# Optimization experiments

Hardware: AMD Instinct MI355X
Metric: run time of the kernel (lower is better)

## Reference

```python
import jax, jax.numpy as jnp
import numpy as np


def setup_inputs() -> dict:
    key = jax.random.key(0)
    ks = jax.random.split(key, 5)
    B, Cin, Ch, H, W, K = 8, 64, 64, 128, 128, 3
    fan_in = (Cin + Ch) * K * K
    return {
        "x": jax.random.normal(ks[0], (B, Cin, H, W), jnp.float32),
        "prev_h": jax.random.normal(ks[1], (B, Ch, H, W), jnp.float32),
        "prev_c": jax.random.normal(ks[2], (B, Ch, H, W), jnp.float32),
        "W_gates": jax.random.normal(ks[3], (4 * Ch, Cin + Ch, K, K), jnp.float32) / np.sqrt(fan_in),
        "b_gates": jax.random.normal(ks[4], (4 * Ch,), jnp.float32) * 0.01,
    }


def reference(x, prev_h, prev_c, W_gates, b_gates):
    # ConvLSTM cell: conv over concat(input, prev_h) -> 4 gates -> gating.
    pad = W_gates.shape[-1] // 2
    stacked = jnp.concatenate([x, prev_h], axis=1)  # [B, Cin+Ch, H, W]
    gates = jax.lax.conv_general_dilated(
        stacked, W_gates,
        window_strides=(1, 1),
        padding=[(pad, pad), (pad, pad)],
        dimension_numbers=("NCHW", "OIHW", "NCHW"),
    ) + b_gates[None, :, None, None]  # [B, 4*Ch, H, W]
    in_gate, remember_gate, out_gate, cell_gate = jnp.split(gates, 4, axis=1)
    in_gate = jax.nn.sigmoid(in_gate)
    remember_gate = jax.nn.sigmoid(remember_gate)
    out_gate = jax.nn.sigmoid(out_gate)
    cell_gate = jnp.tanh(cell_gate)
    cell = in_gate * cell_gate + remember_gate * prev_c
    hidden = out_gate * jnp.tanh(cell)
    return (hidden, cell)
```

## Files before the change

kernel.cpp:

```cpp
#include <hip/hip_runtime.h>

typedef __attribute__((ext_vector_type(8))) short short8;
typedef __attribute__((ext_vector_type(4))) short short4v;
typedef __attribute__((ext_vector_type(4))) float float4v;

#define NPIX_HID 8388608
#define PST 132

__device__ __forceinline__ short f2bf(float f) {
    union { float f; unsigned u; } v; v.f = f;
    unsigned r = (v.u + 0x7FFFu + ((v.u >> 16) & 1u)) >> 16;
    return (short)r;
}

__device__ __forceinline__ float sigmoidf_(float v) { return 1.f / (1.f + __expf(-v)); }
__device__ __forceinline__ float tanhf_(float v)    { return 2.f / (1.f + __expf(-2.f * v)) - 1.f; }

__global__ void wprep(const float* __restrict__ W, short* __restrict__ A) {
    int tid = blockIdx.x * 256 + threadIdx.x;
    if (tid >= 9 * 16 * 256 * 8) return;
    int j   = tid & 7;
    int co  = (tid >> 3) & 255;
    int cig = (tid >> 11) & 15;
    int kk  = tid >> 15;
    int ci  = cig * 8 + j;
    A[tid] = f2bf(W[co * 1152 + ci * 9 + kk]);
}

#define ST_LOAD(P, II)                                                        \
  {                                                                           \
    const int i_ = (II);                                                      \
    P##_act = (i_ < 4224);                                                    \
    const int px_ = i_ % 66;                                                  \
    const int ro_ = i_ / 66;                                                  \
    P##_oct = ro_ & 15;                                                       \
    P##_row = ro_ >> 4;                                                       \
    const int ys_ = y0 + P##_row - 1;                                         \
    const int xs_ = x0 + px_ - 1;                                             \
    P##_px = px_;                                                             \
    P##_ok = P##_act & ((unsigned)ys_ < 128u) & ((unsigned)xs_ < 128u);       \
    const float* src_ = (P##_oct < 8) ? x : ph;                               \
    const float* sp_ = src_ + (P##_ok ?                                       \
        (((b * 64 + (P##_oct & 7) * 8) * 128 + ys_) * 128 + xs_) : 0);        \
    P##_v[0] = sp_[0];        P##_v[1] = sp_[16384];                          \
    P##_v[2] = sp_[2 * 16384]; P##_v[3] = sp_[3 * 16384];                     \
    P##_v[4] = sp_[4 * 16384]; P##_v[5] = sp_[5 * 16384];                     \
    P##_v[6] = sp_[6 * 16384]; P##_v[7] = sp_[7 * 16384];                     \
  }

#define ST_PROC(P)                                                            \
  if (P##_act) {                                                              \
    short4v lo_ = {0,0,0,0}, hi_ = {0,0,0,0};                                 \
    if (P##_ok) {                                                             \
      lo_[0] = f2bf(P##_v[0]); lo_[1] = f2bf(P##_v[1]);                       \
      lo_[2] = f2bf(P##_v[2]); lo_[3] = f2bf(P##_v[3]);                       \
      hi_[0] = f2bf(P##_v[4]); hi_[1] = f2bf(P##_v[5]);                       \
      hi_[2] = f2bf(P##_v[6]); hi_[3] = f2bf(P##_v[7]);                       \
    }                                                                         \
    short* dst_ = &Bs[(P##_row * 66 + P##_px) * PST + P##_oct * 8];           \
    *(short4v*)dst_       = lo_;                                              \
    *(short4v*)(dst_ + 4) = hi_;                                              \
  }

__global__ __launch_bounds__(256, 2) void convlstm_main(
    const float* __restrict__ x, const float* __restrict__ ph,
    const float* __restrict__ pc, const short* __restrict__ aprep,
    const float* __restrict__ bg, float* __restrict__ out)
{
    __shared__ short Bs[4 * 66 * PST];

    const int tid  = threadIdx.x;
    const int lane = tid & 63;
    const int wave = tid >> 6;
    const int l15  = lane & 15;
    const int quad = lane >> 4;

    const int t  = (blockIdx.x & 7) * 128 + (blockIdx.x >> 3);
    const int x0 = (t & 1) * 64;
    const int y0 = ((t >> 1) & 63) * 2;
    const int b  = t >> 7;

    {
        float stA_v[8]; int stA_px, stA_row, stA_oct; bool stA_ok, stA_act;
        float stB_v[8]; int stB_px, stB_row, stB_oct; bool stB_ok, stB_act;
        int ib = tid;
        ST_LOAD(stA, ib);
#pragma unroll 1
        for (int it = 0; it < 16; it += 2) {
            ST_LOAD(stB, ib + 256);
            ST_PROC(stA);
            ST_LOAD(stA, ib + 512);
            ST_PROC(stB);
            ib += 512;
        }
        ST_PROC(stA);
    }
    __syncthreads();

    float4v acc[4][8];
#pragma unroll
    for (int mt = 0; mt < 4; ++mt)
#pragma unroll
        for (int nt = 0; nt < 8; ++nt)
            acc[mt][nt] = (float4v){0.f, 0.f, 0.f, 0.f};

    const short* ap = aprep + quad * 2048 + (wave * 16 + l15) * 8;
    short8 abuf[2][4];
#pragma unroll
    for (int mt = 0; mt < 4; ++mt) abuf[0][mt] = *(const short8*)(ap + mt * 512);

    const short* bb = &Bs[l15 * PST + quad * 8];
    short8 bfr[2][8];
#pragma unroll
    for (int nt = 0; nt < 8; ++nt) {
        const short* bp = bb + (nt >> 2) * (66 * PST) + (nt & 3) * (16 * PST);
        short4v lo = *(const short4v*)bp;
        short4v hi = *(const short4v*)(bp + 4);
        bfr[0][nt] = __builtin_shufflevector(lo, hi, 0, 1, 2, 3, 4, 5, 6, 7);
    }

#pragma unroll 1
    for (int ky = 0; ky < 3; ++ky) {
#pragma unroll 1
        for (int kx = 0; kx < 3; ++kx) {
            const bool lastkx = (ky == 2) & (kx == 2);
            const short* bbn = bb + ((kx == 2) ? 64 * PST : PST);
#pragma unroll
            for (int kc = 0; kc < 4; ++kc) {
                const int cur = kc & 1, nxt = cur ^ 1;
                const bool last = lastkx & (kc == 3);

                const short* apn = last ? ap : (ap + 8192);
#pragma unroll
                for (int mt = 0; mt < 4; ++mt)
                    abuf[nxt][mt] = *(const short8*)(apn + mt * 512);
                ap = apn;

                const short* bq = (kc == 3) ? (lastkx ? bb : bbn) : bb;
                const int kcn = (kc + 1) & 3;
#pragma unroll
                for (int nt = 0; nt < 8; ++nt) {
                    const short* bp = bq + (nt >> 2) * (66 * PST) + (nt & 3) * (16 * PST) + kcn * 32;
                    short4v lo = *(const short4v*)bp;
                    short4v hi = *(const short4v*)(bp + 4);
                    bfr[nxt][nt] = __builtin_shufflevector(lo, hi, 0, 1, 2, 3, 4, 5, 6, 7);
                }

                __builtin_amdgcn_s_setprio(1);
#pragma unroll
                for (int mt = 0; mt < 4; ++mt)
#pragma unroll
                    for (int nt = 0; nt < 8; ++nt)
                        acc[mt][nt] = __builtin_amdgcn_mfma_f32_16x16x32_bf16(
                            abuf[cur][mt], bfr[cur][nt], acc[mt][nt], 0, 0, 0);
                __builtin_amdgcn_s_setprio(0);
            }
            bb = bbn;
        }
    }

    float pcv[8][4];
#pragma unroll
    for (int nt = 0; nt < 8; ++nt) {
        const int y  = y0 + (nt >> 2);
        const int px = x0 + ((nt & 3) << 4) + l15;
#pragma unroll
        for (int r = 0; r < 4; ++r) {
            const int c = wave * 16 + quad * 4 + r;
            pcv[nt][r] = pc[((b * 64 + c) * 128 + y) * 128 + px];
        }
    }
#pragma unroll
    for (int nt = 0; nt < 8; ++nt) {
        const int y  = y0 + (nt >> 2);
        const int px = x0 + ((nt & 3) << 4) + l15;
#pragma unroll
        for (int r = 0; r < 4; ++r) {
            const int c = wave * 16 + quad * 4 + r;
            const float gi = acc[0][nt][r] + bg[c];
            const float gf = acc[1][nt][r] + bg[64 + c];
            const float go = acc[2][nt][r] + bg[128 + c];
            const float gc = acc[3][nt][r] + bg[192 + c];
            const float ig = sigmoidf_(gi);
            const float fg = sigmoidf_(gf);
            const float og = sigmoidf_(go);
            const float cg = tanhf_(gc);
            const int idx = ((b * 64 + c) * 128 + y) * 128 + px;
            const float cell = ig * cg + fg * pcv[nt][r];
            const float hid  = og * tanhf_(cell);
            out[idx] = hid;
            out[NPIX_HID + idx] = cell;
        }
    }
}

extern "C" void kernel_launch(void* const* d_in, const int* in_sizes, int n_in,
                              void* d_out, int out_size, void* d_ws, size_t ws_size,
                              hipStream_t stream) {
    const float* x  = (const float*)d_in[0];
    const float* ph = (const float*)d_in[1];
    const float* pc = (const float*)d_in[2];
    const float* W  = (const float*)d_in[3];
    const float* bg = (const float*)d_in[4];
    float* out = (float*)d_out;
    short* aprep = (short*)d_ws;

    wprep<<<1152, 256, 0, stream>>>(W, aprep);
    convlstm_main<<<1024, 256, 0, stream>>>(x, ph, pc, aprep, bg, out);
}
```

Baseline: 207.1 us.

## Switch conv GEMM to 32x32x16 bf16 MFMA with re-partitioned wave tiling

Replaces the 16x16x32 MFMA tiling (each wave covering 16 channels by all 128 pixels) with 32x32x16 MFMA, so each wave now covers 32 channels by one row of 64 pixels. The weight prep layout is rearranged into 16-wide K chunks to match, and the epilogue channel/pixel mapping is updated for the 32x32 accumulator layout. The aim is fewer MFMA instructions and fewer LDS B-fragment reads per K step. The cost is twice as many K steps per tap with the same A-fragment load count per step, which doubles global weight loads.

New measurement: 219.6 us. 1.06x slower.

```diff
diff --git a/kernel.cpp b/kernel.cpp
--- a/kernel.cpp
+++ b/kernel.cpp
@@ -2,7 +2,7 @@
 
 typedef __attribute__((ext_vector_type(8))) short short8;
 typedef __attribute__((ext_vector_type(4))) short short4v;
-typedef __attribute__((ext_vector_type(4))) float float4v;
+typedef __attribute__((ext_vector_type(16))) float f32x16;
 
 #define NPIX_HID 8388608
 #define PST 132
@@ -18,13 +18,14 @@
 
 __global__ void wprep(const float* __restrict__ W, short* __restrict__ A) {
     int tid = blockIdx.x * 256 + threadIdx.x;
-    if (tid >= 9 * 16 * 256 * 8) return;
-    int j   = tid & 7;
-    int co  = (tid >> 3) & 255;
-    int cig = (tid >> 11) & 15;
-    int kk  = tid >> 15;
-    int ci  = cig * 8 + j;
-    A[tid] = f2bf(W[co * 1152 + ci * 9 + kk]);
+    if (tid >= 294912) return;
+    int j    = tid & 7;
+    int gch  = (tid >> 3) & 255;
+    int half = (tid >> 11) & 1;
+    int kc   = (tid >> 12) & 7;
+    int kk   = tid >> 15;
+    int ci   = kc * 16 + half * 8 + j;
+    A[tid] = f2bf(W[gch * 1152 + ci * 9 + kk]);
 }
 
 #define ST_LOAD(P, II)                                                        \
@@ -72,8 +73,10 @@
     const int tid  = threadIdx.x;
     const int lane = tid & 63;
     const int wave = tid >> 6;
-    const int l15  = lane & 15;
-    const int quad = lane >> 4;
+    const int l31  = lane & 31;
+    const int half = lane >> 5;
+    const int coh  = wave >> 1;
+    const int wy   = wave & 1;
 
     const int t  = (blockIdx.x & 7) * 128 + (blockIdx.x >> 3);
     const int x0 = (t & 1) * 64;
@@ -97,26 +100,28 @@
     }
     __syncthreads();
 
-    float4v acc[4][8];
-#pragma unroll
-    for (int mt = 0; mt < 4; ++mt)
-#pragma unroll
-        for (int nt = 0; nt < 8; ++nt)
-            acc[mt][nt] = (float4v){0.f, 0.f, 0.f, 0.f};
-
-    const short* ap = aprep + quad * 2048 + (wave * 16 + l15) * 8;
+    f32x16 acc[4][2];
+#pragma unroll
+    for (int g = 0; g < 4; ++g)
+#pragma unroll
+        for (int xt = 0; xt < 2; ++xt)
+#pragma unroll
+            for (int r = 0; r < 16; ++r)
+                acc[g][xt][r] = 0.f;
+
+    const short* ap = aprep + half * 2048 + (coh * 32 + l31) * 8;
     short8 abuf[2][4];
 #pragma unroll
-    for (int mt = 0; mt < 4; ++mt) abuf[0][mt] = *(const short8*)(ap + mt * 512);
-
-    const short* bb = &Bs[l15 * PST + quad * 8];
-    short8 bfr[2][8];
-#pragma unroll
-    for (int nt = 0; nt < 8; ++nt) {
-        const short* bp = bb + (nt >> 2) * (66 * PST) + (nt & 3) * (16 * PST);
+    for (int g = 0; g < 4; ++g) abuf[0][g] = *(const short8*)(ap + g * 512);
+
+    const short* bb = &Bs[(wy * 66 + l31) * PST + half * 8];
+    short8 bfr[2][2];
+#pragma unroll
+    for (int xt = 0; xt < 2; ++xt) {
+        const short* bp = bb + xt * (32 * PST);
         short4v lo = *(const short4v*)bp;
         short4v hi = *(const short4v*)(bp + 4);
-        bfr[0][nt] = __builtin_shufflevector(lo, hi, 0, 1, 2, 3, 4, 5, 6, 7);
+        bfr[0][xt] = __builtin_shufflevector(lo, hi, 0, 1, 2, 3, 4, 5, 6, 7);
     }
 
 #pragma unroll 1
@@ -126,67 +131,66 @@
             const bool lastkx = (ky == 2) & (kx == 2);
             const short* bbn = bb + ((kx == 2) ? 64 * PST : PST);
 #pragma unroll
-            for (int kc = 0; kc < 4; ++kc) {
+            for (int kc = 0; kc < 8; ++kc) {
                 const int cur = kc & 1, nxt = cur ^ 1;
-                const bool last = lastkx & (kc == 3);
-
-                const short* apn = last ? ap : (ap + 8192);
-#pragma unroll
-                for (int mt = 0; mt < 4; ++mt)
-                    abuf[nxt][mt] = *(const short8*)(apn + mt * 512);
+                const bool last = lastkx & (kc == 7);
+
+                const short* apn = last ? ap : (ap + 4096);
+#pragma unroll
+                for (int g = 0; g < 4; ++g)
+                    abuf[nxt][g] = *(const short8*)(apn + g * 512);
                 ap = apn;
 
-                const short* bq = (kc == 3) ? (lastkx ? bb : bbn) : bb;
-                const int kcn = (kc + 1) & 3;
-#pragma unroll
-                for (int nt = 0; nt < 8; ++nt) {
-                    const short* bp = bq + (nt >> 2) * (66 * PST) + (nt & 3) * (16 * PST) + kcn * 32;
+                const short* bq = (kc == 7) ? (lastkx ? bb : bbn) : bb;
+                const int kcn = (kc + 1) & 7;
+#pragma unroll
+                for (int xt = 0; xt < 2; ++xt) {
+                    const short* bp = bq + xt * (32 * PST) + kcn * 16;
                     short4v lo = *(const short4v*)bp;
                     short4v hi = *(const short4v*)(bp + 4);
-                    bfr[nxt][nt] = __builtin_shufflevector(lo, hi, 0, 1, 2, 3, 4, 5, 6, 7);
+                    bfr[nxt][xt] = __builtin_shufflevector(lo, hi, 0, 1, 2, 3, 4, 5, 6, 7);
                 }
 
                 __builtin_amdgcn_s_setprio(1);
 #pragma unroll
-                for (int mt = 0; mt < 4; ++mt)
-#pragma unroll
-                    for (int nt = 0; nt < 8; ++nt)
-                        acc[mt][nt] = __builtin_amdgcn_mfma_f32_16x16x32_bf16(
-                            abuf[cur][mt], bfr[cur][nt], acc[mt][nt], 0, 0, 0);
+                for (int g = 0; g < 4; ++g)
+#pragma unroll
+                    for (int xt = 0; xt < 2; ++xt)
+                        acc[g][xt] = __builtin_amdgcn_mfma_f32_32x32x16_bf16(
+                            abuf[cur][g], bfr[cur][xt], acc[g][xt], 0, 0, 0);
                 __builtin_amdgcn_s_setprio(0);
             }
             bb = bbn;
         }
     }
 
-    float pcv[8][4];
-#pragma unroll
-    for (int nt = 0; nt < 8; ++nt) {
-        const int y  = y0 + (nt >> 2);
-        const int px = x0 + ((nt & 3) << 4) + l15;
-#pragma unroll
-        for (int r = 0; r < 4; ++r) {
-            const int c = wave * 16 + quad * 4 + r;
-            pcv[nt][r] = pc[((b * 64 + c) * 128 + y) * 128 + px];
-        }
-    }
-#pragma unroll
-    for (int nt = 0; nt < 8; ++nt) {
-        const int y  = y0 + (nt >> 2);
-        const int px = x0 + ((nt & 3) << 4) + l15;
-#pragma unroll
-        for (int r = 0; r < 4; ++r) {
-            const int c = wave * 16 + quad * 4 + r;
-            const float gi = acc[0][nt][r] + bg[c];
-            const float gf = acc[1][nt][r] + bg[64 + c];
-            const float go = acc[2][nt][r] + bg[128 + c];
-            const float gc = acc[3][nt][r] + bg[192 + c];
+    const int y = y0 + wy;
+    float pcv[2][16];
+#pragma unroll
+    for (int xt = 0; xt < 2; ++xt) {
+        const int px = x0 + xt * 32 + l31;
+#pragma unroll
+        for (int r = 0; r < 16; ++r) {
+            const int c = coh * 32 + (r & 3) + 8 * (r >> 2) + 4 * half;
+            pcv[xt][r] = pc[((b * 64 + c) * 128 + y) * 128 + px];
+        }
+    }
+#pragma unroll
+    for (int xt = 0; xt < 2; ++xt) {
+        const int px = x0 + xt * 32 + l31;
+#pragma unroll
+        for (int r = 0; r < 16; ++r) {
+            const int c = coh * 32 + (r & 3) + 8 * (r >> 2) + 4 * half;
+            const float gi = acc[0][xt][r] + bg[c];
+            const float gf = acc[1][xt][r] + bg[64 + c];
+            const float go = acc[2][xt][r] + bg[128 + c];
+            const float gc = acc[3][xt][r] + bg[192 + c];
             const float ig = sigmoidf_(gi);
             const float fg = sigmoidf_(gf);
             const float og = sigmoidf_(go);
             const float cg = tanhf_(gc);
             const int idx = ((b * 64 + c) * 128 + y) * 128 + px;
-            const float cell = ig * cg + fg * pcv[nt][r];
+            const float cell = ig * cg + fg * pcv[xt][r];
             const float hid  = og * tanhf_(cell);
             out[idx] = hid;
             out[NPIX_HID + idx] = cell;
```

## Pre-convert inputs to bf16 NHWC in separate kernel before conv

Applied to the files above, without the earlier changes.

Adds an xprep kernel that concatenates x and prev_h, converts them to bf16, and transposes them into a channel-last buffer in workspace. The main kernel then stages its halo tile with one 16-byte load per pixel-octet instead of eight strided fp32 loads plus conversion. The cost is an extra kernel launch and a full write and re-read of a bf16 copy of the activations (about 32 MB of extra traffic). The main kernel's staging becomes coalesced and conversion-free, and the halo overlap is now read in half-size bf16.

New measurement: 223.1 us. 7.8% more time.

```diff
diff --git a/kernel.cpp b/kernel.cpp
--- a/kernel.cpp
+++ b/kernel.cpp
@@ -27,45 +27,72 @@
     A[tid] = f2bf(W[co * 1152 + ci * 9 + kk]);
 }
 
-#define ST_LOAD(P, II)                                                        \
+__global__ __launch_bounds__(256) void xprep(const float* __restrict__ x,
+                                             const float* __restrict__ ph,
+                                             short* __restrict__ H) {
+    __shared__ short Ht[64 * 132];
+    const int tid = threadIdx.x;
+    const int t   = blockIdx.x;
+    const int xh  = t & 1;
+    const int y   = (t >> 1) & 127;
+    const int b   = t >> 8;
+    const int xi  = tid & 63;
+    const int cq  = tid >> 6;
+    const int xbase = xh * 64;
+
+#pragma unroll 8
+    for (int it = 0; it < 32; ++it) {
+        const int c = it * 4 + cq;
+        const float* src = (c < 64)
+            ? (x  + (((b * 64 + c)       * 128 + y) * 128 + xbase + xi))
+            : (ph + (((b * 64 + (c & 63)) * 128 + y) * 128 + xbase + xi));
+        Ht[xi * 132 + c] = f2bf(*src);
+    }
+    __syncthreads();
+
+    short* Hb = H + (((b * 128 + y) * 128 + xbase) * 128);
+#pragma unroll
+    for (int r = 0; r < 4; ++r) {
+        const int idx = r * 256 + tid;
+        const int px  = idx >> 4;
+        const int ch  = idx & 15;
+        const short* sp = &Ht[px * 132 + ch * 8];
+        short4v lo = *(const short4v*)sp;
+        short4v hi = *(const short4v*)(sp + 4);
+        *(short8*)(Hb + idx * 8) =
+            __builtin_shufflevector(lo, hi, 0, 1, 2, 3, 4, 5, 6, 7);
+    }
+}
+
+#define XL_LOAD(P, II)                                                        \
   {                                                                           \
     const int i_ = (II);                                                      \
     P##_act = (i_ < 4224);                                                    \
-    const int px_ = i_ % 66;                                                  \
-    const int ro_ = i_ / 66;                                                  \
-    P##_oct = ro_ & 15;                                                       \
-    P##_row = ro_ >> 4;                                                       \
+    const int pr_ = i_ >> 4;                                                  \
+    P##_oct = i_ & 15;                                                        \
+    P##_px  = pr_ % 66;                                                       \
+    P##_row = pr_ / 66;                                                       \
     const int ys_ = y0 + P##_row - 1;                                         \
-    const int xs_ = x0 + px_ - 1;                                             \
-    P##_px = px_;                                                             \
+    const int xs_ = x0 + P##_px - 1;                                          \
     P##_ok = P##_act & ((unsigned)ys_ < 128u) & ((unsigned)xs_ < 128u);       \
-    const float* src_ = (P##_oct < 8) ? x : ph;                               \
-    const float* sp_ = src_ + (P##_ok ?                                       \
-        (((b * 64 + (P##_oct & 7) * 8) * 128 + ys_) * 128 + xs_) : 0);        \
-    P##_v[0] = sp_[0];        P##_v[1] = sp_[16384];                          \
-    P##_v[2] = sp_[2 * 16384]; P##_v[3] = sp_[3 * 16384];                     \
-    P##_v[4] = sp_[4 * 16384]; P##_v[5] = sp_[5 * 16384];                     \
-    P##_v[6] = sp_[6 * 16384]; P##_v[7] = sp_[7 * 16384];                     \
+    const short* hp_ = hsrc + (P##_ok ?                                       \
+        ((((b * 128 + ys_) * 128 + xs_) * 128) + P##_oct * 8) : 0);           \
+    P##_v = *(const short8*)hp_;                                              \
   }
 
-#define ST_PROC(P)                                                            \
+#define XL_PROC(P)                                                            \
   if (P##_act) {                                                              \
-    short4v lo_ = {0,0,0,0}, hi_ = {0,0,0,0};                                 \
-    if (P##_ok) {                                                             \
-      lo_[0] = f2bf(P##_v[0]); lo_[1] = f2bf(P##_v[1]);                       \
-      lo_[2] = f2bf(P##_v[2]); lo_[3] = f2bf(P##_v[3]);                       \
-      hi_[0] = f2bf(P##_v[4]); hi_[1] = f2bf(P##_v[5]);                       \
-      hi_[2] = f2bf(P##_v[6]); hi_[3] = f2bf(P##_v[7]);                       \
-    }                                                                         \
+    short8 v_ = P##_v;                                                        \
+    if (!P##_ok) v_ = (short8){0, 0, 0, 0, 0, 0, 0, 0};                       \
     short* dst_ = &Bs[(P##_row * 66 + P##_px) * PST + P##_oct * 8];           \
-    *(short4v*)dst_       = lo_;                                              \
-    *(short4v*)(dst_ + 4) = hi_;                                              \
+    *(short4v*)dst_       = __builtin_shufflevector(v_, v_, 0, 1, 2, 3);      \
+    *(short4v*)(dst_ + 4) = __builtin_shufflevector(v_, v_, 4, 5, 6, 7);      \
   }
 
 __global__ __launch_bounds__(256, 2) void convlstm_main(
-    const float* __restrict__ x, const float* __restrict__ ph,
-    const float* __restrict__ pc, const short* __restrict__ aprep,
-    const float* __restrict__ bg, float* __restrict__ out)
+    const short* __restrict__ hsrc, const float* __restrict__ pc,
+    const short* __restrict__ aprep, const float* __restrict__ bg,
+    float* __restrict__ out)
 {
     __shared__ short Bs[4 * 66 * PST];
 
@@ -81,19 +108,19 @@
     const int b  = t >> 7;
 
     {
-        float stA_v[8]; int stA_px, stA_row, stA_oct; bool stA_ok, stA_act;
-        float stB_v[8]; int stB_px, stB_row, stB_oct; bool stB_ok, stB_act;
+        short8 stA_v; int stA_px, stA_row, stA_oct; bool stA_ok, stA_act;
+        short8 stB_v; int stB_px, stB_row, stB_oct; bool stB_ok, stB_act;
         int ib = tid;
-        ST_LOAD(stA, ib);
+        XL_LOAD(stA, ib);
 #pragma unroll 1
         for (int it = 0; it < 16; it += 2) {
-            ST_LOAD(stB, ib + 256);
-            ST_PROC(stA);
-            ST_LOAD(stA, ib + 512);
-            ST_PROC(stB);
+            XL_LOAD(stB, ib + 256);
+            XL_PROC(stA);
+            XL_LOAD(stA, ib + 512);
+            XL_PROC(stB);
             ib += 512;
         }
-        ST_PROC(stA);
+        XL_PROC(stA);
     }
     __syncthreads();
 
@@ -204,7 +231,9 @@
     const float* bg = (const float*)d_in[4];
     float* out = (float*)d_out;
     short* aprep = (short*)d_ws;
+    short* H     = (short*)d_ws + 294912;
 
     wprep<<<1152, 256, 0, stream>>>(W, aprep);
-    convlstm_main<<<1024, 256, 0, stream>>>(x, ph, pc, aprep, bg, out);
-}
+    xprep<<<2048, 256, 0, stream>>>(x, ph, H);
+    convlstm_main<<<1024, 256, 0, stream>>>(H, pc, aprep, bg, out);
+}
```
